# Optimization experiments

Measured on AMD Instinct MI355X. Metric: run time of the kernel, lower is better.

The kernel has to match this reference:

```python
import jax, jax.numpy as jnp
import numpy as np

N = 100000      # nodes
E = 3200000     # edges (avg degree 32)
F_IN = 16       # node_feature_size
R1, R2, R3 = 8, 16, 8   # gcn hidden sizes
N1 = 32                  # mlp hidden


def _lin(k, fan_in, shape):
    s = 1.0 / np.sqrt(fan_in)
    return jax.random.uniform(k, shape, minval=-s, maxval=s, dtype=jnp.float32)


def setup_inputs() -> dict:
    key = jax.random.key(0)
    ks = jax.random.split(key, 16)
    x = jax.random.normal(ks[0], (N, F_IN), dtype=jnp.float32)
    edge_index = jax.random.randint(ks[1], (2, E), 0, N, dtype=jnp.int64)
    return {
        "x": x,
        "edge_index": edge_index,
        # GraphConv k: out = mean_agg(x_j) @ W_rel + b + x @ W_root  (PyG GraphConv, lin_root bias=False)
        "W_rel1": _lin(ks[2], F_IN, (F_IN, R1)), "b1": _lin(ks[3], F_IN, (R1,)), "W_root1": _lin(ks[4], F_IN, (F_IN, R1)),
        "W_rel2": _lin(ks[5], R1, (R1, R2)),   "b2": _lin(ks[6], R1, (R2,)),   "W_root2": _lin(ks[7], R1, (R1, R2)),
        "W_rel3": _lin(ks[8], R2, (R2, R3)),   "b3": _lin(ks[9], R2, (R3,)),   "W_root3": _lin(ks[10], R2, (R2, R3)),
        "fc1_W": _lin(ks[11], R3, (R3, N1)), "fc1_b": _lin(ks[12], R3, (N1,)),
        "fc2_W": _lin(ks[13], N1, (N1, 1)),  "fc2_b": _lin(ks[14], N1, (1,)),
    }


def _graph_conv(x, src, dst, W_rel, b, W_root):
    # message: gather source features; aggregate: mean over incoming edges at dst
    n = x.shape[0]
    msg_sum = jax.ops.segment_sum(x[src], dst, num_segments=n)          # [N, F]
    cnt = jax.ops.segment_sum(jnp.ones(src.shape, x.dtype), dst, num_segments=n)
    mean = msg_sum / jnp.maximum(cnt, 1.0)[:, None]
    return mean @ W_rel + b + x @ W_root


def reference(x, edge_index, W_rel1, b1, W_root1, W_rel2, b2, W_root2,
              W_rel3, b3, W_root3, fc1_W, fc1_b, fc2_W, fc2_b):
    src, dst = edge_index[0], edge_index[1]
    h = jax.nn.sigmoid(_graph_conv(x, src, dst, W_rel1, b1, W_root1))
    h = jax.nn.sigmoid(_graph_conv(h, src, dst, W_rel2, b2, W_root2))
    h = jax.nn.sigmoid(_graph_conv(h, src, dst, W_rel3, b3, W_root3))
    h = jax.nn.sigmoid(h @ fc1_W + fc1_b)
    return h @ fc2_W + fc2_b   # [N, 1]
```

## Files before the change

### kernel.cpp

```cpp
#include <hip/hip_runtime.h>
#include <math.h>


#define CHUNK  8192
#define BW     128
#define MAXB   6144
#define MAXNB  800
#define MAXBLK 512

typedef _Float16 half8 __attribute__((ext_vector_type(8)));

static __device__ __forceinline__ float sigmoidf_(float x) {
    return 1.0f / (1.0f + expf(-x));
}

static __device__ __forceinline__ int scan256_excl(int v, int* s) {
    int tid = threadIdx.x;
    s[tid] = v;
    for (int off = 1; off < 256; off <<= 1) {
        __syncthreads();
        int t = (tid >= off) ? s[tid - off] : 0;
        __syncthreads();
        s[tid] += t;
    }
    __syncthreads();
    return s[tid] - v;
}

static __device__ __forceinline__ void gather_mean8(
    const half8* __restrict__ t, const int* __restrict__ csr,
    int rs, int d, float* s) {
#pragma unroll
    for (int c = 0; c < 8; ++c) s[c] = 0.0f;
    int e = 0;
    for (; e + 4 <= d; e += 4) {
        int4 ci = *(const int4*)(csr + rs + e);
        half8 v0 = t[ci.x]; half8 v1 = t[ci.y];
        half8 v2 = t[ci.z]; half8 v3 = t[ci.w];
#pragma unroll
        for (int c = 0; c < 8; ++c)
            s[c] += ((float)v0[c] + (float)v1[c]) + ((float)v2[c] + (float)v3[c]);
    }
    for (; e < d; ++e) {
        half8 v = t[csr[rs + e]];
#pragma unroll
        for (int c = 0; c < 8; ++c) s[c] += (float)v[c];
    }
    float inv = 1.0f / (float)(d > 0 ? d : 1);
#pragma unroll
    for (int c = 0; c < 8; ++c) s[c] *= inv;
}

__global__ __launch_bounds__(256)
void transform1_kernel(const float* __restrict__ x, const float* __restrict__ Wrel,
                       const float* __restrict__ bias, const float* __restrict__ Wroot,
                       _Float16* __restrict__ t1, _Float16* __restrict__ z1, int n) {
    __shared__ float sWr[128], sWo[128], sb[8];
    int tid = threadIdx.x;
    if (tid < 128) { sWr[tid] = Wrel[tid]; sWo[tid] = Wroot[tid]; }
    if (tid < 8) sb[tid] = bias[tid];
    __syncthreads();
    int node = blockIdx.x * 256 + tid;
    if (node >= n) return;
    const float4* x4 = (const float4*)x;
    float xv[16];
#pragma unroll
    for (int k = 0; k < 4; ++k) {
        float4 v = x4[node * 4 + k];
        xv[4 * k] = v.x; xv[4 * k + 1] = v.y; xv[4 * k + 2] = v.z; xv[4 * k + 3] = v.w;
    }
    float ta[8], za[8];
#pragma unroll
    for (int j = 0; j < 8; ++j) { ta[j] = 0.0f; za[j] = sb[j]; }
#pragma unroll
    for (int f = 0; f < 16; ++f) {
        float xf = xv[f];
#pragma unroll
        for (int j = 0; j < 8; ++j) {
            ta[j] += xf * sWr[f * 8 + j];
            za[j] += xf * sWo[f * 8 + j];
        }
    }
    half8 th, zh;
#pragma unroll
    for (int j = 0; j < 8; ++j) { th[j] = (_Float16)ta[j]; zh[j] = (_Float16)za[j]; }
    ((half8*)t1)[node] = th;
    ((half8*)z1)[node] = zh;
}

__global__ __launch_bounds__(256)
void bin_sort_kernel(const int* __restrict__ src, const int* __restrict__ dst,
                     unsigned* __restrict__ packed, int* __restrict__ counts_bm,
                     int* __restrict__ lstart_bm, int E, int NB) {
    __shared__ int s_hist[MAXNB];
    __shared__ int s_cur[MAXNB];
    __shared__ unsigned s_pk[CHUNK];
    __shared__ int s_scan[256];
    int tid = threadIdx.x, blk = blockIdx.x;
    for (int i = tid; i < NB; i += 256) s_hist[i] = 0;
    __syncthreads();

    int base = blk * CHUNK;
    int cnt = E - base; if (cnt > CHUNK) cnt = CHUNK;

    if (cnt == CHUNK) {
        const int4* d4 = (const int4*)(dst + base);
#pragma unroll
        for (int k = 0; k < CHUNK / 1024; ++k) {
            int4 d = d4[k * 256 + tid];
            atomicAdd(&s_hist[d.x >> 7], 1);
            atomicAdd(&s_hist[d.y >> 7], 1);
            atomicAdd(&s_hist[d.z >> 7], 1);
            atomicAdd(&s_hist[d.w >> 7], 1);
        }
    } else {
        for (int i = tid; i < cnt; i += 256) atomicAdd(&s_hist[dst[base + i] >> 7], 1);
    }
    __syncthreads();

    int per = (NB + 255) / 256;
    int st = tid * per;
    int lsum = 0;
    for (int j = 0; j < per; ++j)
        if (st + j < NB) lsum += s_hist[st + j];
    int excl = scan256_excl(lsum, s_scan);
    int run = excl;
    for (int j = 0; j < per; ++j)
        if (st + j < NB) { s_cur[st + j] = run; run += s_hist[st + j]; }
    __syncthreads();

    if (cnt == CHUNK) {
        const int4* d4 = (const int4*)(dst + base);
        const int4* s4 = (const int4*)(src + base);
#pragma unroll
        for (int k = 0; k < CHUNK / 1024; ++k) {
            int4 d = d4[k * 256 + tid];
            int4 s = s4[k * 256 + tid];
            int dd[4] = {d.x, d.y, d.z, d.w};
            int ss[4] = {s.x, s.y, s.z, s.w};
#pragma unroll
            for (int j = 0; j < 4; ++j) {
                int pos = atomicAdd(&s_cur[dd[j] >> 7], 1);
                s_pk[pos] = ((unsigned)(dd[j] & 127) << 17) | (unsigned)ss[j];
            }
        }
    } else {
        for (int i = tid; i < cnt; i += 256) {
            int d = dst[base + i], s = src[base + i];
            int pos = atomicAdd(&s_cur[d >> 7], 1);
            s_pk[pos] = ((unsigned)(d & 127) << 17) | (unsigned)s;
        }
    }
    __syncthreads();

    for (int i = tid; i < cnt; i += 256) packed[base + i] = s_pk[i];
    for (int i = tid; i < NB; i += 256) {
        int h = s_hist[i];
        counts_bm[blk * NB + i] = h;
        lstart_bm[blk * NB + i] = s_cur[i] - h;
    }
}

__global__ __launch_bounds__(256)
void transpose2_kernel(const int* __restrict__ a, int* __restrict__ at,
                       const int* __restrict__ b, int* __restrict__ bt,
                       int rows, int cols) {
    __shared__ int ta[32][33];
    __shared__ int tb[32][33];
    int tx = threadIdx.x & 31, ty = threadIdx.x >> 5;
    int r0 = blockIdx.y * 32, c0 = blockIdx.x * 32;
#pragma unroll
    for (int k = 0; k < 4; ++k) {
        int r = r0 + ty + 8 * k, c = c0 + tx;
        if (r < rows && c < cols) {
            ta[ty + 8 * k][tx] = a[r * cols + c];
            tb[ty + 8 * k][tx] = b[r * cols + c];
        }
    }
    __syncthreads();
#pragma unroll
    for (int k = 0; k < 4; ++k) {
        int c = c0 + ty + 8 * k, r = r0 + tx;
        if (c < cols && r < rows) {
            at[c * rows + r] = ta[tx][ty + 8 * k];
            bt[c * rows + r] = tb[tx][ty + 8 * k];
        }
    }
}

__global__ __launch_bounds__(256)
void btot_kernel(const int* __restrict__ counts_t, int* __restrict__ btot, int NBLK) {
    __shared__ int s_scan[256];
    int b = blockIdx.x, tid = threadIdx.x;
    int v = 0;
    for (int i = tid; i < NBLK; i += 256) v += counts_t[b * NBLK + i];
    scan256_excl(v, s_scan);
    if (tid == 255) btot[b] = s_scan[255];
}

__global__ __launch_bounds__(1024)
void bscan_kernel(const int* __restrict__ btot, int* __restrict__ bstart, int NB) {
    __shared__ int lds[1024];
    int tid = threadIdx.x;
    int v = (tid < NB) ? (((btot[tid] + 3) & ~3) + 512) : 0;
    lds[tid] = v;
    for (int off = 1; off < 1024; off <<= 1) {
        __syncthreads();
        int t = (tid >= off) ? lds[tid - off] : 0;
        __syncthreads();
        lds[tid] += t;
    }
    __syncthreads();
    if (tid < NB) bstart[tid] = lds[tid] - v;
}

__global__ __launch_bounds__(256)
void bucket_sort_kernel(const unsigned* __restrict__ packed,
                        const int* __restrict__ counts_t,
                        const int* __restrict__ lstart_t,
                        const int* __restrict__ bstart,
                        int* __restrict__ csr_src, int* __restrict__ deg,
                        int* __restrict__ rowstart, int N, int NB, int NBLK) {
    __shared__ int s_cnt[MAXBLK], s_lst[MAXBLK], s_off[MAXBLK];
    __shared__ unsigned s_p[MAXB];
    __shared__ int s_out[MAXB];
    __shared__ int h[BW], hs[BW], curb[BW];
    __shared__ int s_scan[256];
    __shared__ int s_tot, s_ptot;
    int b = blockIdx.x, tid = threadIdx.x;
    int beg = bstart[b];

    for (int i = tid; i < NBLK; i += 256) {
        s_cnt[i] = counts_t[b * NBLK + i];
        s_lst[i] = lstart_t[b * NBLK + i];
    }
    __syncthreads();

    int per = (NBLK + 255) / 256;
    int st = tid * per;
    int lsum = 0;
    for (int j = 0; j < per; ++j)
        if (st + j < NBLK) lsum += s_cnt[st + j];
    int excl = scan256_excl(lsum, s_scan);
    if (tid == 255) s_tot = s_scan[255];
    int run = excl;
    for (int j = 0; j < per; ++j)
        if (st + j < NBLK) { s_off[st + j] = run; run += s_cnt[st + j]; }
    __syncthreads();
    int cnt = s_tot; if (cnt > MAXB) cnt = MAXB;

    for (int blk = tid; blk < NBLK; blk += 256) {
        int c = s_cnt[blk], o = s_off[blk];
        const unsigned* p = packed + (size_t)blk * CHUNK + s_lst[blk];
        for (int j = 0; j < c; ++j) s_p[o + j] = p[j];
    }
    if (tid < BW) h[tid] = 0;
    __syncthreads();

    for (int i = tid; i < cnt; i += 256) atomicAdd(&h[s_p[i] >> 17], 1);
    __syncthreads();
    if (tid == 0) {
        int acc = 0;
        for (int i = 0; i < BW; ++i) { hs[i] = acc; acc += (h[i] + 3) & ~3; }
        s_ptot = acc;
    }
    __syncthreads();
    if (tid < BW) {
        curb[tid] = hs[tid];
        int node = b * BW + tid;
        if (node < N) { deg[node] = h[tid]; rowstart[node] = beg + hs[tid]; }
    }
    __syncthreads();
    for (int i = tid; i < cnt; i += 256) {
        unsigned p = s_p[i];
        int pos = atomicAdd(&curb[p >> 17], 1);
        s_out[pos] = (int)(p & 0x1FFFF);
    }
    __syncthreads();
    int ptot = s_ptot; if (ptot > MAXB) ptot = MAXB;
    for (int i = tid; i < ptot; i += 256) csr_src[beg + i] = s_out[i];
}

__global__ __launch_bounds__(256)
void agg1_kernel(const _Float16* __restrict__ t1, const _Float16* __restrict__ z1,
                 const int* __restrict__ rowstart, const int* __restrict__ deg,
                 const int* __restrict__ csr, _Float16* __restrict__ h1, int n) {
    int node = blockIdx.x * 256 + threadIdx.x;
    if (node >= n) return;
    float s[8];
    gather_mean8((const half8*)t1, csr, rowstart[node], deg[node], s);
    half8 z = ((const half8*)z1)[node];
    half8 o;
#pragma unroll
    for (int c = 0; c < 8; ++c) o[c] = (_Float16)sigmoidf_(s[c] + (float)z[c]);
    ((half8*)h1)[node] = o;
}

__global__ __launch_bounds__(256)
void gcn2_fused_kernel(const _Float16* __restrict__ h1,
                       const int* __restrict__ rowstart, const int* __restrict__ deg,
                       const int* __restrict__ csr,
                       const float* __restrict__ W2r, const float* __restrict__ b2,
                       const float* __restrict__ W2o,
                       const float* __restrict__ W3r, const float* __restrict__ b3,
                       const float* __restrict__ W3o,
                       _Float16* __restrict__ t3, _Float16* __restrict__ z3, int n) {
    __shared__ float sW2r[128], sW2o[128], sW3r[128], sW3o[128], sb2[16], sb3[8];
    int tid = threadIdx.x;
    if (tid < 128) {
        sW2r[tid] = W2r[tid]; sW2o[tid] = W2o[tid];
        sW3r[tid] = W3r[tid]; sW3o[tid] = W3o[tid];
    }
    if (tid < 16) sb2[tid] = b2[tid];
    if (tid < 8) sb3[tid] = b3[tid];
    __syncthreads();
    int node = blockIdx.x * 256 + tid;
    if (node >= n) return;

    float m[8];
    gather_mean8((const half8*)h1, csr, rowstart[node], deg[node], m);
    half8 sf = ((const half8*)h1)[node];
    float x8[8];
#pragma unroll
    for (int c = 0; c < 8; ++c) x8[c] = (float)sf[c];

    float v16[16];
#pragma unroll
    for (int j = 0; j < 16; ++j) {
        float a = sb2[j];
#pragma unroll
        for (int f = 0; f < 8; ++f)
            a += m[f] * sW2r[f * 16 + j] + x8[f] * sW2o[f * 16 + j];
        v16[j] = sigmoidf_(a);
    }
    float ta[8], za[8];
#pragma unroll
    for (int j = 0; j < 8; ++j) { ta[j] = 0.0f; za[j] = sb3[j]; }
#pragma unroll
    for (int f = 0; f < 16; ++f) {
        float hv = v16[f];
#pragma unroll
        for (int j = 0; j < 8; ++j) {
            ta[j] += hv * sW3r[f * 8 + j];
            za[j] += hv * sW3o[f * 8 + j];
        }
    }
    half8 th, zh;
#pragma unroll
    for (int j = 0; j < 8; ++j) { th[j] = (_Float16)ta[j]; zh[j] = (_Float16)za[j]; }
    ((half8*)t3)[node] = th;
    ((half8*)z3)[node] = zh;
}

__global__ __launch_bounds__(256)
void agg3_mlp_kernel(const _Float16* __restrict__ t3, const _Float16* __restrict__ z3,
                     const int* __restrict__ rowstart, const int* __restrict__ deg,
                     const int* __restrict__ csr,
                     const float* __restrict__ fc1W, const float* __restrict__ fc1b,
                     const float* __restrict__ fc2W, const float* __restrict__ fc2b,
                     float* __restrict__ out, int n) {
    __shared__ float sW1[256], sb1[32], sW2[32];
    __shared__ float sb2_;
    int tid = threadIdx.x;
    if (tid < 256) sW1[tid] = fc1W[tid];
    if (tid < 32) { sb1[tid] = fc1b[tid]; sW2[tid] = fc2W[tid]; }
    if (tid == 0) sb2_ = fc2b[0];
    __syncthreads();
    int node = blockIdx.x * 256 + tid;
    if (node >= n) return;

    float s[8];
    gather_mean8((const half8*)t3, csr, rowstart[node], deg[node], s);
    half8 z = ((const half8*)z3)[node];
    float h[8];
#pragma unroll
    for (int c = 0; c < 8; ++c) h[c] = sigmoidf_(s[c] + (float)z[c]);

    float acc = sb2_;
#pragma unroll
    for (int j = 0; j < 32; ++j) {
        float a = sb1[j];
#pragma unroll
        for (int f = 0; f < 8; ++f) a += h[f] * sW1[f * 32 + j];
        acc += sW2[j] * sigmoidf_(a);
    }
    out[node] = acc;
}

extern "C" void kernel_launch(void* const* d_in, const int* in_sizes, int n_in,
                              void* d_out, int out_size, void* d_ws, size_t ws_size,
                              hipStream_t stream) {
    const float* x      = (const float*)d_in[0];
    const int*   ei     = (const int*)d_in[1];
    const float* Wrel1  = (const float*)d_in[2];
    const float* b1     = (const float*)d_in[3];
    const float* Wroot1 = (const float*)d_in[4];
    const float* Wrel2  = (const float*)d_in[5];
    const float* b2     = (const float*)d_in[6];
    const float* Wroot2 = (const float*)d_in[7];
    const float* Wrel3  = (const float*)d_in[8];
    const float* b3     = (const float*)d_in[9];
    const float* Wroot3 = (const float*)d_in[10];
    const float* fc1W   = (const float*)d_in[11];
    const float* fc1b   = (const float*)d_in[12];
    const float* fc2W   = (const float*)d_in[13];
    const float* fc2b   = (const float*)d_in[14];
    float* out = (float*)d_out;

    const int N = in_sizes[0] / 16;
    const int E = in_sizes[1] / 2;
    const int* e_src = ei;
    const int* e_dst = ei + E;

    const int NB   = (N + BW - 1) / BW;
    const int NBLK = (E + CHUNK - 1) / CHUNK;

    char* ws = (char*)d_ws;
    size_t off = 0;
    auto alloc = [&](size_t bytes) { char* p = ws + off; off += (bytes + 15) & ~size_t(15); return p; };
    unsigned* packed   = (unsigned*)alloc((size_t)NBLK * CHUNK * 4);
    int* counts_bm     = (int*)alloc((size_t)NBLK * NB * 4);
    int* lstart_bm     = (int*)alloc((size_t)NBLK * NB * 4);
    int* counts_t      = (int*)alloc((size_t)NBLK * NB * 4);
    int* lstart_t      = (int*)alloc((size_t)NBLK * NB * 4);
    int* btot          = (int*)alloc((size_t)NB * 4);
    int* bstart        = (int*)alloc((size_t)NB * 4);
    int* csr_src       = (int*)alloc(((size_t)E + (size_t)NB * 516) * 4);
    int* deg           = (int*)alloc((size_t)N * 4);
    int* rowstart      = (int*)alloc((size_t)N * 4);
    _Float16* t1       = (_Float16*)alloc((size_t)N * 8 * 2);
    _Float16* z1       = (_Float16*)alloc((size_t)N * 8 * 2);
    _Float16* h1       = (_Float16*)alloc((size_t)N * 8 * 2);
    _Float16* t3       = (_Float16*)alloc((size_t)N * 8 * 2);
    _Float16* z3       = (_Float16*)alloc((size_t)N * 8 * 2);

    const int nbN = (N + 255) / 256;

    transform1_kernel<<<nbN, 256, 0, stream>>>(x, Wrel1, b1, Wroot1, t1, z1, N);

    bin_sort_kernel<<<NBLK, 256, 0, stream>>>(e_src, e_dst, packed, counts_bm, lstart_bm, E, NB);
    dim3 tgrid((NB + 31) / 32, (NBLK + 31) / 32);
    transpose2_kernel<<<tgrid, 256, 0, stream>>>(counts_bm, counts_t, lstart_bm, lstart_t, NBLK, NB);
    btot_kernel<<<NB, 256, 0, stream>>>(counts_t, btot, NBLK);
    bscan_kernel<<<1, 1024, 0, stream>>>(btot, bstart, NB);
    bucket_sort_kernel<<<NB, 256, 0, stream>>>(packed, counts_t, lstart_t, bstart,
                                               csr_src, deg, rowstart, N, NB, NBLK);

    agg1_kernel<<<nbN, 256, 0, stream>>>(t1, z1, rowstart, deg, csr_src, h1, N);
    gcn2_fused_kernel<<<nbN, 256, 0, stream>>>(h1, rowstart, deg, csr_src,
                                               Wrel2, b2, Wroot2, Wrel3, b3, Wroot3, t3, z3, N);
    agg3_mlp_kernel<<<nbN, 256, 0, stream>>>(t3, z3, rowstart, deg, csr_src,
                                             fc1W, fc1b, fc2W, fc2b, out, N);
}
```

Measured before the change: 232.6 us.

## Replace full CSR sort with bucket-only scatter and LDS atomic aggregation

Measured after the change: 672.5 us. 189% more time.

```diff
diff --git a/kernel.cpp b/kernel.cpp
--- a/kernel.cpp
+++ b/kernel.cpp
@@ -4,9 +4,9 @@
 
 #define CHUNK  8192
 #define BW     128
-#define MAXB   6144
 #define MAXNB  800
 #define MAXBLK 512
+#define AST    9
 
 typedef _Float16 half8 __attribute__((ext_vector_type(8)));
 
@@ -27,30 +27,6 @@
     return s[tid] - v;
 }
 
-static __device__ __forceinline__ void gather_mean8(
-    const half8* __restrict__ t, const int* __restrict__ csr,
-    int rs, int d, float* s) {
-#pragma unroll
-    for (int c = 0; c < 8; ++c) s[c] = 0.0f;
-    int e = 0;
-    for (; e + 4 <= d; e += 4) {
-        int4 ci = *(const int4*)(csr + rs + e);
-        half8 v0 = t[ci.x]; half8 v1 = t[ci.y];
-        half8 v2 = t[ci.z]; half8 v3 = t[ci.w];
-#pragma unroll
-        for (int c = 0; c < 8; ++c)
-            s[c] += ((float)v0[c] + (float)v1[c]) + ((float)v2[c] + (float)v3[c]);
-    }
-    for (; e < d; ++e) {
-        half8 v = t[csr[rs + e]];
-#pragma unroll
-        for (int c = 0; c < 8; ++c) s[c] += (float)v[c];
-    }
-    float inv = 1.0f / (float)(d > 0 ? d : 1);
-#pragma unroll
-    for (int c = 0; c < 8; ++c) s[c] *= inv;
-}
-
 __global__ __launch_bounds__(256)
 void transform1_kernel(const float* __restrict__ x, const float* __restrict__ Wrel,
                        const float* __restrict__ bias, const float* __restrict__ Wroot,
@@ -89,20 +65,14 @@
 }
 
 __global__ __launch_bounds__(256)
-void bin_sort_kernel(const int* __restrict__ src, const int* __restrict__ dst,
-                     unsigned* __restrict__ packed, int* __restrict__ counts_bm,
-                     int* __restrict__ lstart_bm, int E, int NB) {
+void hist_kernel(const int* __restrict__ dst, int* __restrict__ counts_bm,
+                 int E, int NB) {
     __shared__ int s_hist[MAXNB];
-    __shared__ int s_cur[MAXNB];
-    __shared__ unsigned s_pk[CHUNK];
-    __shared__ int s_scan[256];
     int tid = threadIdx.x, blk = blockIdx.x;
     for (int i = tid; i < NB; i += 256) s_hist[i] = 0;
     __syncthreads();
-
     int base = blk * CHUNK;
     int cnt = E - base; if (cnt > CHUNK) cnt = CHUNK;
-
     if (cnt == CHUNK) {
         const int4* d4 = (const int4*)(dst + base);
 #pragma unroll
@@ -117,84 +87,26 @@
         for (int i = tid; i < cnt; i += 256) atomicAdd(&s_hist[dst[base + i] >> 7], 1);
     }
     __syncthreads();
-
-    int per = (NB + 255) / 256;
+    for (int i = tid; i < NB; i += 256) counts_bm[blk * NB + i] = s_hist[i];
+}
+
+__global__ __launch_bounds__(256)
+void btot_scan_kernel(const int* __restrict__ counts_bm, int* __restrict__ rawstart_t,
+                      int* __restrict__ btot, int NB, int NBLK) {
+    __shared__ int s_scan[256];
+    __shared__ int s_c[MAXBLK];
+    int b = blockIdx.x, tid = threadIdx.x;
+    for (int i = tid; i < NBLK; i += 256) s_c[i] = counts_bm[i * NB + b];
+    __syncthreads();
+    int per = (NBLK + 255) / 256;
     int st = tid * per;
     int lsum = 0;
     for (int j = 0; j < per; ++j)
-        if (st + j < NB) lsum += s_hist[st + j];
+        if (st + j < NBLK) lsum += s_c[st + j];
     int excl = scan256_excl(lsum, s_scan);
     int run = excl;
     for (int j = 0; j < per; ++j)
-        if (st + j < NB) { s_cur[st + j] = run; run += s_hist[st + j]; }
-    __syncthreads();
-
-    if (cnt == CHUNK) {
-        const int4* d4 = (const int4*)(dst + base);
-        const int4* s4 = (const int4*)(src + base);
-#pragma unroll
-        for (int k = 0; k < CHUNK / 1024; ++k) {
-            int4 d = d4[k * 256 + tid];
-            int4 s = s4[k * 256 + tid];
-            int dd[4] = {d.x, d.y, d.z, d.w};
-            int ss[4] = {s.x, s.y, s.z, s.w};
-#pragma unroll
-            for (int j = 0; j < 4; ++j) {
-                int pos = atomicAdd(&s_cur[dd[j] >> 7], 1);
-                s_pk[pos] = ((unsigned)(dd[j] & 127) << 17) | (unsigned)ss[j];
-            }
-        }
-    } else {
-        for (int i = tid; i < cnt; i += 256) {
-            int d = dst[base + i], s = src[base + i];
-            int pos = atomicAdd(&s_cur[d >> 7], 1);
-            s_pk[pos] = ((unsigned)(d & 127) << 17) | (unsigned)s;
-        }
-    }
-    __syncthreads();
-
-    for (int i = tid; i < cnt; i += 256) packed[base + i] = s_pk[i];
-    for (int i = tid; i < NB; i += 256) {
-        int h = s_hist[i];
-        counts_bm[blk * NB + i] = h;
-        lstart_bm[blk * NB + i] = s_cur[i] - h;
-    }
-}
-
-__global__ __launch_bounds__(256)
-void transpose2_kernel(const int* __restrict__ a, int* __restrict__ at,
-                       const int* __restrict__ b, int* __restrict__ bt,
-                       int rows, int cols) {
-    __shared__ int ta[32][33];
-    __shared__ int tb[32][33];
-    int tx = threadIdx.x & 31, ty = threadIdx.x >> 5;
-    int r0 = blockIdx.y * 32, c0 = blockIdx.x * 32;
-#pragma unroll
-    for (int k = 0; k < 4; ++k) {
-        int r = r0 + ty + 8 * k, c = c0 + tx;
-        if (r < rows && c < cols) {
-            ta[ty + 8 * k][tx] = a[r * cols + c];
-            tb[ty + 8 * k][tx] = b[r * cols + c];
-        }
-    }
-    __syncthreads();
-#pragma unroll
-    for (int k = 0; k < 4; ++k) {
-        int c = c0 + ty + 8 * k, r = r0 + tx;
-        if (c < cols && r < rows) {
-            at[c * rows + r] = ta[tx][ty + 8 * k];
-            bt[c * rows + r] = tb[tx][ty + 8 * k];
-        }
-    }
-}
-
-__global__ __launch_bounds__(256)
-void btot_kernel(const int* __restrict__ counts_t, int* __restrict__ btot, int NBLK) {
-    __shared__ int s_scan[256];
-    int b = blockIdx.x, tid = threadIdx.x;
-    int v = 0;
-    for (int i = tid; i < NBLK; i += 256) v += counts_t[b * NBLK + i];
-    scan256_excl(v, s_scan);
+        if (st + j < NBLK) { rawstart_t[b * NBLK + st + j] = run; run += s_c[st + j]; }
     if (tid == 255) btot[b] = s_scan[255];
 }
 
@@ -202,7 +114,7 @@
 void bscan_kernel(const int* __restrict__ btot, int* __restrict__ bstart, int NB) {
     __shared__ int lds[1024];
     int tid = threadIdx.x;
-    int v = (tid < NB) ? (((btot[tid] + 3) & ~3) + 512) : 0;
+    int v = (tid < NB) ? ((btot[tid] + 3) & ~3) : 0;
     lds[tid] = v;
     for (int off = 1; off < 1024; off <<= 1) {
         __syncthreads();
@@ -215,176 +127,219 @@
 }
 
 __global__ __launch_bounds__(256)
-void bucket_sort_kernel(const unsigned* __restrict__ packed,
-                        const int* __restrict__ counts_t,
-                        const int* __restrict__ lstart_t,
-                        const int* __restrict__ bstart,
-                        int* __restrict__ csr_src, int* __restrict__ deg,
-                        int* __restrict__ rowstart, int N, int NB, int NBLK) {
-    __shared__ int s_cnt[MAXBLK], s_lst[MAXBLK], s_off[MAXBLK];
-    __shared__ unsigned s_p[MAXB];
-    __shared__ int s_out[MAXB];
-    __shared__ int h[BW], hs[BW], curb[BW];
-    __shared__ int s_scan[256];
-    __shared__ int s_tot, s_ptot;
-    int b = blockIdx.x, tid = threadIdx.x;
-    int beg = bstart[b];
-
-    for (int i = tid; i < NBLK; i += 256) {
-        s_cnt[i] = counts_t[b * NBLK + i];
-        s_lst[i] = lstart_t[b * NBLK + i];
-    }
-    __syncthreads();
-
-    int per = (NBLK + 255) / 256;
-    int st = tid * per;
-    int lsum = 0;
-    for (int j = 0; j < per; ++j)
-        if (st + j < NBLK) lsum += s_cnt[st + j];
-    int excl = scan256_excl(lsum, s_scan);
-    if (tid == 255) s_tot = s_scan[255];
-    int run = excl;
-    for (int j = 0; j < per; ++j)
-        if (st + j < NBLK) { s_off[st + j] = run; run += s_cnt[st + j]; }
-    __syncthreads();
-    int cnt = s_tot; if (cnt > MAXB) cnt = MAXB;
-
-    for (int blk = tid; blk < NBLK; blk += 256) {
-        int c = s_cnt[blk], o = s_off[blk];
-        const unsigned* p = packed + (size_t)blk * CHUNK + s_lst[blk];
-        for (int j = 0; j < c; ++j) s_p[o + j] = p[j];
-    }
-    if (tid < BW) h[tid] = 0;
-    __syncthreads();
-
-    for (int i = tid; i < cnt; i += 256) atomicAdd(&h[s_p[i] >> 17], 1);
-    __syncthreads();
-    if (tid == 0) {
-        int acc = 0;
-        for (int i = 0; i < BW; ++i) { hs[i] = acc; acc += (h[i] + 3) & ~3; }
-        s_ptot = acc;
+void scatter_kernel(const int* __restrict__ src, const int* __restrict__ dst,
+                    const int* __restrict__ rawstart_t, const int* __restrict__ bstart,
+                    unsigned* __restrict__ stage, int E, int NB, int NBLK) {
+    __shared__ int s_cur[MAXNB];
+    int tid = threadIdx.x, blk = blockIdx.x;
+    for (int i = tid; i < NB; i += 256)
+        s_cur[i] = bstart[i] + rawstart_t[i * NBLK + blk];
+    __syncthreads();
+    int base = blk * CHUNK;
+    int cnt = E - base; if (cnt > CHUNK) cnt = CHUNK;
+    if (cnt == CHUNK) {
+        const int4* d4 = (const int4*)(dst + base);
+        const int4* s4 = (const int4*)(src + base);
+#pragma unroll
+        for (int k = 0; k < CHUNK / 1024; ++k) {
+            int4 d = d4[k * 256 + tid];
+            int4 s = s4[k * 256 + tid];
+            int dd[4] = {d.x, d.y, d.z, d.w};
+            int ss[4] = {s.x, s.y, s.z, s.w};
+#pragma unroll
+            for (int j = 0; j < 4; ++j) {
+                int pos = atomicAdd(&s_cur[dd[j] >> 7], 1);
+                stage[pos] = ((unsigned)(dd[j] & 127) << 17) | (unsigned)ss[j];
+            }
+        }
+    } else {
+        for (int i = tid; i < cnt; i += 256) {
+            int d = dst[base + i], s = src[base + i];
+            int pos = atomicAdd(&s_cur[d >> 7], 1);
+            stage[pos] = ((unsigned)(d & 127) << 17) | (unsigned)s;
+        }
+    }
+}
+
+static __device__ __forceinline__ void edge_add8(float* __restrict__ acc, unsigned p,
+                                                 const half8* __restrict__ t) {
+    int s  = (int)(p & 0x1FFFFu);
+    int ld = (int)(p >> 17);
+    half8 v = t[s];
+    float* a = acc + ld * AST;
+#pragma unroll
+    for (int c = 0; c < 8; ++c) atomicAdd(&a[c], (float)v[c]);
+}
+
+__global__ __launch_bounds__(256)
+void agg1_kernel(const _Float16* __restrict__ t1, const _Float16* __restrict__ z1,
+                 const unsigned* __restrict__ stage, const int* __restrict__ bstart,
+                 const int* __restrict__ btot, _Float16* __restrict__ h1,
+                 float* __restrict__ invdeg, int N) {
+    __shared__ float acc[BW * AST];
+    __shared__ int scnt[BW];
+    int tid = threadIdx.x, b = blockIdx.x;
+    for (int i = tid; i < BW * AST; i += 256) acc[i] = 0.0f;
+    if (tid < BW) scnt[tid] = 0;
+    __syncthreads();
+    int beg = bstart[b], tot = btot[b];
+    const half8* t = (const half8*)t1;
+    const uint4* st4 = (const uint4*)(stage + beg);
+    int n4 = tot >> 2;
+    for (int i = tid; i < n4; i += 256) {
+        uint4 p = st4[i];
+        edge_add8(acc, p.x, t); atomicAdd(&scnt[p.x >> 17], 1);
+        edge_add8(acc, p.y, t); atomicAdd(&scnt[p.y >> 17], 1);
+        edge_add8(acc, p.z, t); atomicAdd(&scnt[p.z >> 17], 1);
+        edge_add8(acc, p.w, t); atomicAdd(&scnt[p.w >> 17], 1);
+    }
+    int r = (n4 << 2) + tid;
+    if (r < tot) {
+        unsigned p = stage[beg + r];
+        edge_add8(acc, p, t); atomicAdd(&scnt[p >> 17], 1);
     }
     __syncthreads();
     if (tid < BW) {
-        curb[tid] = hs[tid];
         int node = b * BW + tid;
-        if (node < N) { deg[node] = h[tid]; rowstart[node] = beg + hs[tid]; }
-    }
-    __syncthreads();
-    for (int i = tid; i < cnt; i += 256) {
-        unsigned p = s_p[i];
-        int pos = atomicAdd(&curb[p >> 17], 1);
-        s_out[pos] = (int)(p & 0x1FFFF);
-    }
-    __syncthreads();
-    int ptot = s_ptot; if (ptot > MAXB) ptot = MAXB;
-    for (int i = tid; i < ptot; i += 256) csr_src[beg + i] = s_out[i];
-}
-
-__global__ __launch_bounds__(256)
-void agg1_kernel(const _Float16* __restrict__ t1, const _Float16* __restrict__ z1,
-                 const int* __restrict__ rowstart, const int* __restrict__ deg,
-                 const int* __restrict__ csr, _Float16* __restrict__ h1, int n) {
-    int node = blockIdx.x * 256 + threadIdx.x;
-    if (node >= n) return;
-    float s[8];
-    gather_mean8((const half8*)t1, csr, rowstart[node], deg[node], s);
-    half8 z = ((const half8*)z1)[node];
-    half8 o;
-#pragma unroll
-    for (int c = 0; c < 8; ++c) o[c] = (_Float16)sigmoidf_(s[c] + (float)z[c]);
-    ((half8*)h1)[node] = o;
-}
-
-__global__ __launch_bounds__(256)
-void gcn2_fused_kernel(const _Float16* __restrict__ h1,
-                       const int* __restrict__ rowstart, const int* __restrict__ deg,
-                       const int* __restrict__ csr,
-                       const float* __restrict__ W2r, const float* __restrict__ b2,
-                       const float* __restrict__ W2o,
-                       const float* __restrict__ W3r, const float* __restrict__ b3,
-                       const float* __restrict__ W3o,
-                       _Float16* __restrict__ t3, _Float16* __restrict__ z3, int n) {
+        if (node < N) {
+            int c = scnt[tid];
+            float inv = 1.0f / (float)(c > 0 ? c : 1);
+            half8 z = ((const half8*)z1)[node];
+            half8 o;
+#pragma unroll
+            for (int j = 0; j < 8; ++j)
+                o[j] = (_Float16)sigmoidf_(acc[tid * AST + j] * inv + (float)z[j]);
+            ((half8*)h1)[node] = o;
+            invdeg[node] = inv;
+        }
+    }
+}
+
+__global__ __launch_bounds__(256)
+void agg2_kernel(const _Float16* __restrict__ h1, const unsigned* __restrict__ stage,
+                 const int* __restrict__ bstart, const int* __restrict__ btot,
+                 const float* __restrict__ invdeg,
+                 const float* __restrict__ W2r, const float* __restrict__ b2,
+                 const float* __restrict__ W2o,
+                 const float* __restrict__ W3r, const float* __restrict__ b3,
+                 const float* __restrict__ W3o,
+                 _Float16* __restrict__ t3, _Float16* __restrict__ z3, int N) {
+    __shared__ float acc[BW * AST];
     __shared__ float sW2r[128], sW2o[128], sW3r[128], sW3o[128], sb2[16], sb3[8];
-    int tid = threadIdx.x;
+    int tid = threadIdx.x, b = blockIdx.x;
     if (tid < 128) {
         sW2r[tid] = W2r[tid]; sW2o[tid] = W2o[tid];
         sW3r[tid] = W3r[tid]; sW3o[tid] = W3o[tid];
     }
     if (tid < 16) sb2[tid] = b2[tid];
     if (tid < 8) sb3[tid] = b3[tid];
-    __syncthreads();
-    int node = blockIdx.x * 256 + tid;
-    if (node >= n) return;
-
-    float m[8];
-    gather_mean8((const half8*)h1, csr, rowstart[node], deg[node], m);
-    half8 sf = ((const half8*)h1)[node];
-    float x8[8];
-#pragma unroll
-    for (int c = 0; c < 8; ++c) x8[c] = (float)sf[c];
-
-    float v16[16];
-#pragma unroll
-    for (int j = 0; j < 16; ++j) {
-        float a = sb2[j];
-#pragma unroll
-        for (int f = 0; f < 8; ++f)
-            a += m[f] * sW2r[f * 16 + j] + x8[f] * sW2o[f * 16 + j];
-        v16[j] = sigmoidf_(a);
-    }
-    float ta[8], za[8];
-#pragma unroll
-    for (int j = 0; j < 8; ++j) { ta[j] = 0.0f; za[j] = sb3[j]; }
-#pragma unroll
-    for (int f = 0; f < 16; ++f) {
-        float hv = v16[f];
-#pragma unroll
-        for (int j = 0; j < 8; ++j) {
-            ta[j] += hv * sW3r[f * 8 + j];
-            za[j] += hv * sW3o[f * 8 + j];
-        }
-    }
-    half8 th, zh;
-#pragma unroll
-    for (int j = 0; j < 8; ++j) { th[j] = (_Float16)ta[j]; zh[j] = (_Float16)za[j]; }
-    ((half8*)t3)[node] = th;
-    ((half8*)z3)[node] = zh;
-}
-
-__global__ __launch_bounds__(256)
-void agg3_mlp_kernel(const _Float16* __restrict__ t3, const _Float16* __restrict__ z3,
-                     const int* __restrict__ rowstart, const int* __restrict__ deg,
-                     const int* __restrict__ csr,
-                     const float* __restrict__ fc1W, const float* __restrict__ fc1b,
-                     const float* __restrict__ fc2W, const float* __restrict__ fc2b,
-                     float* __restrict__ out, int n) {
+    for (int i = tid; i < BW * AST; i += 256) acc[i] = 0.0f;
+    __syncthreads();
+    int beg = bstart[b], tot = btot[b];
+    const half8* t = (const half8*)h1;
+    const uint4* st4 = (const uint4*)(stage + beg);
+    int n4 = tot >> 2;
+    for (int i = tid; i < n4; i += 256) {
+        uint4 p = st4[i];
+        edge_add8(acc, p.x, t);
+        edge_add8(acc, p.y, t);
+        edge_add8(acc, p.z, t);
+        edge_add8(acc, p.w, t);
+    }
+    int r = (n4 << 2) + tid;
+    if (r < tot) edge_add8(acc, stage[beg + r], t);
+    __syncthreads();
+    if (tid < BW) {
+        int node = b * BW + tid;
+        if (node < N) {
+            float inv = invdeg[node];
+            float m[8];
+#pragma unroll
+            for (int f = 0; f < 8; ++f) m[f] = acc[tid * AST + f] * inv;
+            half8 sf = ((const half8*)h1)[node];
+            float x8[8];
+#pragma unroll
+            for (int f = 0; f < 8; ++f) x8[f] = (float)sf[f];
+            float v16[16];
+#pragma unroll
+            for (int j = 0; j < 16; ++j) {
+                float a = sb2[j];
+#pragma unroll
+                for (int f = 0; f < 8; ++f)
+                    a += m[f] * sW2r[f * 16 + j] + x8[f] * sW2o[f * 16 + j];
+                v16[j] = sigmoidf_(a);
+            }
+            float ta[8], za[8];
+#pragma unroll
+            for (int j = 0; j < 8; ++j) { ta[j] = 0.0f; za[j] = sb3[j]; }
+#pragma unroll
+            for (int f = 0; f < 16; ++f) {
+                float hv = v16[f];
+#pragma unroll
+                for (int j = 0; j < 8; ++j) {
+                    ta[j] += hv * sW3r[f * 8 + j];
+                    za[j] += hv * sW3o[f * 8 + j];
+                }
+            }
+            half8 th, zh;
+#pragma unroll
+            for (int j = 0; j < 8; ++j) { th[j] = (_Float16)ta[j]; zh[j] = (_Float16)za[j]; }
+            ((half8*)t3)[node] = th;
+            ((half8*)z3)[node] = zh;
+        }
+    }
+}
+
+__global__ __launch_bounds__(256)
+void agg3_kernel(const _Float16* __restrict__ t3, const _Float16* __restrict__ z3,
+                 const unsigned* __restrict__ stage, const int* __restrict__ bstart,
+                 const int* __restrict__ btot, const float* __restrict__ invdeg,
+                 const float* __restrict__ fc1W, const float* __restrict__ fc1b,
+                 const float* __restrict__ fc2W, const float* __restrict__ fc2b,
+                 float* __restrict__ out, int N) {
+    __shared__ float acc[BW * AST];
     __shared__ float sW1[256], sb1[32], sW2[32];
     __shared__ float sb2_;
-    int tid = threadIdx.x;
+    int tid = threadIdx.x, b = blockIdx.x;
     if (tid < 256) sW1[tid] = fc1W[tid];
     if (tid < 32) { sb1[tid] = fc1b[tid]; sW2[tid] = fc2W[tid]; }
     if (tid == 0) sb2_ = fc2b[0];
-    __syncthreads();
-    int node = blockIdx.x * 256 + tid;
-    if (node >= n) return;
-
-    float s[8];
-    gather_mean8((const half8*)t3, csr, rowstart[node], deg[node], s);
-    half8 z = ((const half8*)z3)[node];
-    float h[8];
-#pragma unroll
-    for (int c = 0; c < 8; ++c) h[c] = sigmoidf_(s[c] + (float)z[c]);
-
-    float acc = sb2_;
-#pragma unroll
-    for (int j = 0; j < 32; ++j) {
-        float a = sb1[j];
-#pragma unroll
-        for (int f = 0; f < 8; ++f) a += h[f] * sW1[f * 32 + j];
-        acc += sW2[j] * sigmoidf_(a);
-    }
-    out[node] = acc;
+    for (int i = tid; i < BW * AST; i += 256) acc[i] = 0.0f;
+    __syncthreads();
+    int beg = bstart[b], tot = btot[b];
+    const half8* t = (const half8*)t3;
+    const uint4* st4 = (const uint4*)(stage + beg);
+    int n4 = tot >> 2;
+    for (int i = tid; i < n4; i += 256) {
+        uint4 p = st4[i];
+        edge_add8(acc, p.x, t);
+        edge_add8(acc, p.y, t);
+        edge_add8(acc, p.z, t);
+        edge_add8(acc, p.w, t);
+    }
+    int r = (n4 << 2) + tid;
+    if (r < tot) edge_add8(acc, stage[beg + r], t);
+    __syncthreads();
+    if (tid < BW) {
+        int node = b * BW + tid;
+        if (node < N) {
+            float inv = invdeg[node];
+            half8 z = ((const half8*)z3)[node];
+            float h[8];
+#pragma unroll
+            for (int c = 0; c < 8; ++c)
+                h[c] = sigmoidf_(acc[tid * AST + c] * inv + (float)z[c]);
+            float a2 = sb2_;
+#pragma unroll
+            for (int j = 0; j < 32; ++j) {
+                float a = sb1[j];
+#pragma unroll
+                for (int f = 0; f < 8; ++f) a += h[f] * sW1[f * 32 + j];
+                a2 += sW2[j] * sigmoidf_(a);
+            }
+            out[node] = a2;
+        }
+    }
 }
 
 extern "C" void kernel_launch(void* const* d_in, const int* in_sizes, int n_in,
@@ -418,16 +373,12 @@
     char* ws = (char*)d_ws;
     size_t off = 0;
     auto alloc = [&](size_t bytes) { char* p = ws + off; off += (bytes + 15) & ~size_t(15); return p; };
-    unsigned* packed   = (unsigned*)alloc((size_t)NBLK * CHUNK * 4);
+    unsigned* stage    = (unsigned*)alloc(((size_t)E + 4 * (size_t)NB + 64) * 4);
     int* counts_bm     = (int*)alloc((size_t)NBLK * NB * 4);
-    int* lstart_bm     = (int*)alloc((size_t)NBLK * NB * 4);
-    int* counts_t      = (int*)alloc((size_t)NBLK * NB * 4);
-    int* lstart_t      = (int*)alloc((size_t)NBLK * NB * 4);
+    int* rawstart_t    = (int*)alloc((size_t)NB * NBLK * 4);
     int* btot          = (int*)alloc((size_t)NB * 4);
     int* bstart        = (int*)alloc((size_t)NB * 4);
-    int* csr_src       = (int*)alloc(((size_t)E + (size_t)NB * 516) * 4);
-    int* deg           = (int*)alloc((size_t)N * 4);
-    int* rowstart      = (int*)alloc((size_t)N * 4);
+    float* invdeg      = (float*)alloc((size_t)N * 4);
     _Float16* t1       = (_Float16*)alloc((size_t)N * 8 * 2);
     _Float16* z1       = (_Float16*)alloc((size_t)N * 8 * 2);
     _Float16* h1       = (_Float16*)alloc((size_t)N * 8 * 2);
@@ -438,17 +389,14 @@
 
     transform1_kernel<<<nbN, 256, 0, stream>>>(x, Wrel1, b1, Wroot1, t1, z1, N);
 
-    bin_sort_kernel<<<NBLK, 256, 0, stream>>>(e_src, e_dst, packed, counts_bm, lstart_bm, E, NB);
-    dim3 tgrid((NB + 31) / 32, (NBLK + 31) / 32);
-    transpose2_kernel<<<tgrid, 256, 0, stream>>>(counts_bm, counts_t, lstart_bm, lstart_t, NBLK, NB);
-    btot_kernel<<<NB, 256, 0, stream>>>(counts_t, btot, NBLK);
+    hist_kernel<<<NBLK, 256, 0, stream>>>(e_dst, counts_bm, E, NB);
+    btot_scan_kernel<<<NB, 256, 0, stream>>>(counts_bm, rawstart_t, btot, NB, NBLK);
     bscan_kernel<<<1, 1024, 0, stream>>>(btot, bstart, NB);
-    bucket_sort_kernel<<<NB, 256, 0, stream>>>(packed, counts_t, lstart_t, bstart,
-                                               csr_src, deg, rowstart, N, NB, NBLK);
-
-    agg1_kernel<<<nbN, 256, 0, stream>>>(t1, z1, rowstart, deg, csr_src, h1, N);
-    gcn2_fused_kernel<<<nbN, 256, 0, stream>>>(h1, rowstart, deg, csr_src,
-                                               Wrel2, b2, Wroot2, Wrel3, b3, Wroot3, t3, z3, N);
-    agg3_mlp_kernel<<<nbN, 256, 0, stream>>>(t3, z3, rowstart, deg, csr_src,
-                                             fc1W, fc1b, fc2W, fc2b, out, N);
-}
+    scatter_kernel<<<NBLK, 256, 0, stream>>>(e_src, e_dst, rawstart_t, bstart, stage, E, NB, NBLK);
+
+    agg1_kernel<<<NB, 256, 0, stream>>>(t1, z1, stage, bstart, btot, h1, invdeg, N);
+    agg2_kernel<<<NB, 256, 0, stream>>>(h1, stage, bstart, btot, invdeg,
+                                        Wrel2, b2, Wroot2, Wrel3, b3, Wroot3, t3, z3, N);
+    agg3_kernel<<<NB, 256, 0, stream>>>(t3, z3, stage, bstart, btot, invdeg,
+                                        fc1W, fc1b, fc2W, fc2b, out, N);
+}
```

## Replace two-level bucket sort CSR build with global atomic counting sort

Applied to the files above, without the earlier changes.

Result: slower. 554.4 us (+138.4%).

```diff
diff --git a/kernel.cpp b/kernel.cpp
--- a/kernel.cpp
+++ b/kernel.cpp
@@ -2,11 +2,7 @@
 #include <math.h>
 
 
-#define CHUNK  8192
-#define BW     128
-#define MAXB   6144
-#define MAXNB  800
-#define MAXBLK 512
+#define ECHUNK 4096
 
 typedef _Float16 half8 __attribute__((ext_vector_type(8)));
 
@@ -54,7 +50,8 @@
 __global__ __launch_bounds__(256)
 void transform1_kernel(const float* __restrict__ x, const float* __restrict__ Wrel,
                        const float* __restrict__ bias, const float* __restrict__ Wroot,
-                       _Float16* __restrict__ t1, _Float16* __restrict__ z1, int n) {
+                       _Float16* __restrict__ t1, _Float16* __restrict__ z1,
+                       int* __restrict__ deg, int n) {
     __shared__ float sWr[128], sWo[128], sb[8];
     int tid = threadIdx.x;
     if (tid < 128) { sWr[tid] = Wrel[tid]; sWo[tid] = Wroot[tid]; }
@@ -62,6 +59,7 @@
     __syncthreads();
     int node = blockIdx.x * 256 + tid;
     if (node >= n) return;
+    deg[node] = 0;
     const float4* x4 = (const float4*)x;
     float xv[16];
 #pragma unroll
@@ -89,196 +87,94 @@
 }
 
 __global__ __launch_bounds__(256)
-void bin_sort_kernel(const int* __restrict__ src, const int* __restrict__ dst,
-                     unsigned* __restrict__ packed, int* __restrict__ counts_bm,
-                     int* __restrict__ lstart_bm, int E, int NB) {
-    __shared__ int s_hist[MAXNB];
-    __shared__ int s_cur[MAXNB];
-    __shared__ unsigned s_pk[CHUNK];
+void deg_count_kernel(const int* __restrict__ dst, int* __restrict__ deg, int E) {
+    int base = blockIdx.x * ECHUNK;
+    int tid = threadIdx.x;
+    int cnt = E - base; if (cnt > ECHUNK) cnt = ECHUNK;
+    if (cnt == ECHUNK) {
+        const int4* d4 = (const int4*)(dst + base);
+#pragma unroll
+        for (int k = 0; k < ECHUNK / 1024; ++k) {
+            int4 d = d4[k * 256 + tid];
+            atomicAdd(&deg[d.x], 1); atomicAdd(&deg[d.y], 1);
+            atomicAdd(&deg[d.z], 1); atomicAdd(&deg[d.w], 1);
+        }
+    } else {
+        for (int i = tid; i < cnt; i += 256) atomicAdd(&deg[dst[base + i]], 1);
+    }
+}
+
+__global__ __launch_bounds__(256)
+void blocksum_kernel(const int* __restrict__ deg, int* __restrict__ bsum, int N) {
+    __shared__ int s[256];
+    int tid = threadIdx.x;
+    int i = blockIdx.x * 256 + tid;
+    int p = (i < N) ? ((deg[i] + 3) & ~3) : 0;
+    s[tid] = p;
+    for (int off = 128; off > 0; off >>= 1) {
+        __syncthreads();
+        if (tid < off) s[tid] += s[tid + off];
+    }
+    __syncthreads();
+    if (tid == 0) bsum[blockIdx.x] = s[0];
+}
+
+__global__ __launch_bounds__(512)
+void bscan_kernel(const int* __restrict__ bsum, int* __restrict__ bbase, int nb) {
+    __shared__ int lds[512];
+    int tid = threadIdx.x;
+    int v = (tid < nb) ? bsum[tid] : 0;
+    lds[tid] = v;
+    for (int off = 1; off < 512; off <<= 1) {
+        __syncthreads();
+        int t = (tid >= off) ? lds[tid - off] : 0;
+        __syncthreads();
+        lds[tid] += t;
+    }
+    __syncthreads();
+    if (tid < nb) bbase[tid] = lds[tid] - v;
+}
+
+__global__ __launch_bounds__(256)
+void rowwrite_kernel(const int* __restrict__ deg, const int* __restrict__ bbase,
+                     int* __restrict__ rowstart, int* __restrict__ cur, int N) {
     __shared__ int s_scan[256];
-    int tid = threadIdx.x, blk = blockIdx.x;
-    for (int i = tid; i < NB; i += 256) s_hist[i] = 0;
-    __syncthreads();
-
-    int base = blk * CHUNK;
-    int cnt = E - base; if (cnt > CHUNK) cnt = CHUNK;
-
-    if (cnt == CHUNK) {
-        const int4* d4 = (const int4*)(dst + base);
-#pragma unroll
-        for (int k = 0; k < CHUNK / 1024; ++k) {
-            int4 d = d4[k * 256 + tid];
-            atomicAdd(&s_hist[d.x >> 7], 1);
-            atomicAdd(&s_hist[d.y >> 7], 1);
-            atomicAdd(&s_hist[d.z >> 7], 1);
-            atomicAdd(&s_hist[d.w >> 7], 1);
-        }
-    } else {
-        for (int i = tid; i < cnt; i += 256) atomicAdd(&s_hist[dst[base + i] >> 7], 1);
-    }
-    __syncthreads();
-
-    int per = (NB + 255) / 256;
-    int st = tid * per;
-    int lsum = 0;
-    for (int j = 0; j < per; ++j)
-        if (st + j < NB) lsum += s_hist[st + j];
-    int excl = scan256_excl(lsum, s_scan);
-    int run = excl;
-    for (int j = 0; j < per; ++j)
-        if (st + j < NB) { s_cur[st + j] = run; run += s_hist[st + j]; }
-    __syncthreads();
-
-    if (cnt == CHUNK) {
+    int tid = threadIdx.x;
+    int i = blockIdx.x * 256 + tid;
+    int p = (i < N) ? ((deg[i] + 3) & ~3) : 0;
+    int excl = scan256_excl(p, s_scan);
+    if (i < N) {
+        int r = bbase[blockIdx.x] + excl;
+        rowstart[i] = r;
+        cur[i] = r;
+    }
+}
+
+__global__ __launch_bounds__(256)
+void scatter_kernel(const int* __restrict__ src, const int* __restrict__ dst,
+                    int* __restrict__ cur, int* __restrict__ csr, int E) {
+    int base = blockIdx.x * ECHUNK;
+    int tid = threadIdx.x;
+    int cnt = E - base; if (cnt > ECHUNK) cnt = ECHUNK;
+    if (cnt == ECHUNK) {
         const int4* d4 = (const int4*)(dst + base);
         const int4* s4 = (const int4*)(src + base);
 #pragma unroll
-        for (int k = 0; k < CHUNK / 1024; ++k) {
+        for (int k = 0; k < ECHUNK / 1024; ++k) {
             int4 d = d4[k * 256 + tid];
             int4 s = s4[k * 256 + tid];
-            int dd[4] = {d.x, d.y, d.z, d.w};
-            int ss[4] = {s.x, s.y, s.z, s.w};
-#pragma unroll
-            for (int j = 0; j < 4; ++j) {
-                int pos = atomicAdd(&s_cur[dd[j] >> 7], 1);
-                s_pk[pos] = ((unsigned)(dd[j] & 127) << 17) | (unsigned)ss[j];
-            }
+            int pos;
+            pos = atomicAdd(&cur[d.x], 1); csr[pos] = s.x;
+            pos = atomicAdd(&cur[d.y], 1); csr[pos] = s.y;
+            pos = atomicAdd(&cur[d.z], 1); csr[pos] = s.z;
+            pos = atomicAdd(&cur[d.w], 1); csr[pos] = s.w;
         }
     } else {
         for (int i = tid; i < cnt; i += 256) {
-            int d = dst[base + i], s = src[base + i];
-            int pos = atomicAdd(&s_cur[d >> 7], 1);
-            s_pk[pos] = ((unsigned)(d & 127) << 17) | (unsigned)s;
-        }
-    }
-    __syncthreads();
-
-    for (int i = tid; i < cnt; i += 256) packed[base + i] = s_pk[i];
-    for (int i = tid; i < NB; i += 256) {
-        int h = s_hist[i];
-        counts_bm[blk * NB + i] = h;
-        lstart_bm[blk * NB + i] = s_cur[i] - h;
-    }
-}
-
-__global__ __launch_bounds__(256)
-void transpose2_kernel(const int* __restrict__ a, int* __restrict__ at,
-                       const int* __restrict__ b, int* __restrict__ bt,
-                       int rows, int cols) {
-    __shared__ int ta[32][33];
-    __shared__ int tb[32][33];
-    int tx = threadIdx.x & 31, ty = threadIdx.x >> 5;
-    int r0 = blockIdx.y * 32, c0 = blockIdx.x * 32;
-#pragma unroll
-    for (int k = 0; k < 4; ++k) {
-        int r = r0 + ty + 8 * k, c = c0 + tx;
-        if (r < rows && c < cols) {
-            ta[ty + 8 * k][tx] = a[r * cols + c];
-            tb[ty + 8 * k][tx] = b[r * cols + c];
-        }
-    }
-    __syncthreads();
-#pragma unroll
-    for (int k = 0; k < 4; ++k) {
-        int c = c0 + ty + 8 * k, r = r0 + tx;
-        if (c < cols && r < rows) {
-            at[c * rows + r] = ta[tx][ty + 8 * k];
-            bt[c * rows + r] = tb[tx][ty + 8 * k];
-        }
-    }
-}
-
-__global__ __launch_bounds__(256)
-void btot_kernel(const int* __restrict__ counts_t, int* __restrict__ btot, int NBLK) {
-    __shared__ int s_scan[256];
-    int b = blockIdx.x, tid = threadIdx.x;
-    int v = 0;
-    for (int i = tid; i < NBLK; i += 256) v += counts_t[b * NBLK + i];
-    scan256_excl(v, s_scan);
-    if (tid == 255) btot[b] = s_scan[255];
-}
-
-__global__ __launch_bounds__(1024)
-void bscan_kernel(const int* __restrict__ btot, int* __restrict__ bstart, int NB) {
-    __shared__ int lds[1024];
-    int tid = threadIdx.x;
-    int v = (tid < NB) ? (((btot[tid] + 3) & ~3) + 512) : 0;
-    lds[tid] = v;
-    for (int off = 1; off < 1024; off <<= 1) {
-        __syncthreads();
-        int t = (tid >= off) ? lds[tid - off] : 0;
-        __syncthreads();
-        lds[tid] += t;
-    }
-    __syncthreads();
-    if (tid < NB) bstart[tid] = lds[tid] - v;
-}
-
-__global__ __launch_bounds__(256)
-void bucket_sort_kernel(const unsigned* __restrict__ packed,
-                        const int* __restrict__ counts_t,
-                        const int* __restrict__ lstart_t,
-                        const int* __restrict__ bstart,
-                        int* __restrict__ csr_src, int* __restrict__ deg,
-                        int* __restrict__ rowstart, int N, int NB, int NBLK) {
-    __shared__ int s_cnt[MAXBLK], s_lst[MAXBLK], s_off[MAXBLK];
-    __shared__ unsigned s_p[MAXB];
-    __shared__ int s_out[MAXB];
-    __shared__ int h[BW], hs[BW], curb[BW];
-    __shared__ int s_scan[256];
-    __shared__ int s_tot, s_ptot;
-    int b = blockIdx.x, tid = threadIdx.x;
-    int beg = bstart[b];
-
-    for (int i = tid; i < NBLK; i += 256) {
-        s_cnt[i] = counts_t[b * NBLK + i];
-        s_lst[i] = lstart_t[b * NBLK + i];
-    }
-    __syncthreads();
-
-    int per = (NBLK + 255) / 256;
-    int st = tid * per;
-    int lsum = 0;
-    for (int j = 0; j < per; ++j)
-        if (st + j < NBLK) lsum += s_cnt[st + j];
-    int excl = scan256_excl(lsum, s_scan);
-    if (tid == 255) s_tot = s_scan[255];
-    int run = excl;
-    for (int j = 0; j < per; ++j)
-        if (st + j < NBLK) { s_off[st + j] = run; run += s_cnt[st + j]; }
-    __syncthreads();
-    int cnt = s_tot; if (cnt > MAXB) cnt = MAXB;
-
-    for (int blk = tid; blk < NBLK; blk += 256) {
-        int c = s_cnt[blk], o = s_off[blk];
-        const unsigned* p = packed + (size_t)blk * CHUNK + s_lst[blk];
-        for (int j = 0; j < c; ++j) s_p[o + j] = p[j];
-    }
-    if (tid < BW) h[tid] = 0;
-    __syncthreads();
-
-    for (int i = tid; i < cnt; i += 256) atomicAdd(&h[s_p[i] >> 17], 1);
-    __syncthreads();
-    if (tid == 0) {
-        int acc = 0;
-        for (int i = 0; i < BW; ++i) { hs[i] = acc; acc += (h[i] + 3) & ~3; }
-        s_ptot = acc;
-    }
-    __syncthreads();
-    if (tid < BW) {
-        curb[tid] = hs[tid];
-        int node = b * BW + tid;
-        if (node < N) { deg[node] = h[tid]; rowstart[node] = beg + hs[tid]; }
-    }
-    __syncthreads();
-    for (int i = tid; i < cnt; i += 256) {
-        unsigned p = s_p[i];
-        int pos = atomicAdd(&curb[p >> 17], 1);
-        s_out[pos] = (int)(p & 0x1FFFF);
-    }
-    __syncthreads();
-    int ptot = s_ptot; if (ptot > MAXB) ptot = MAXB;
-    for (int i = tid; i < ptot; i += 256) csr_src[beg + i] = s_out[i];
+            int pos = atomicAdd(&cur[dst[base + i]], 1);
+            csr[pos] = src[base + i];
+        }
+    }
 }
 
 __global__ __launch_bounds__(256)
@@ -412,43 +308,35 @@
     const int* e_src = ei;
     const int* e_dst = ei + E;
 
-    const int NB   = (N + BW - 1) / BW;
-    const int NBLK = (E + CHUNK - 1) / CHUNK;
+    const int nbN = (N + 255) / 256;
+    const int nbE = (E + ECHUNK - 1) / ECHUNK;
 
     char* ws = (char*)d_ws;
     size_t off = 0;
     auto alloc = [&](size_t bytes) { char* p = ws + off; off += (bytes + 15) & ~size_t(15); return p; };
-    unsigned* packed   = (unsigned*)alloc((size_t)NBLK * CHUNK * 4);
-    int* counts_bm     = (int*)alloc((size_t)NBLK * NB * 4);
-    int* lstart_bm     = (int*)alloc((size_t)NBLK * NB * 4);
-    int* counts_t      = (int*)alloc((size_t)NBLK * NB * 4);
-    int* lstart_t      = (int*)alloc((size_t)NBLK * NB * 4);
-    int* btot          = (int*)alloc((size_t)NB * 4);
-    int* bstart        = (int*)alloc((size_t)NB * 4);
-    int* csr_src       = (int*)alloc(((size_t)E + (size_t)NB * 516) * 4);
-    int* deg           = (int*)alloc((size_t)N * 4);
-    int* rowstart      = (int*)alloc((size_t)N * 4);
-    _Float16* t1       = (_Float16*)alloc((size_t)N * 8 * 2);
-    _Float16* z1       = (_Float16*)alloc((size_t)N * 8 * 2);
-    _Float16* h1       = (_Float16*)alloc((size_t)N * 8 * 2);
-    _Float16* t3       = (_Float16*)alloc((size_t)N * 8 * 2);
-    _Float16* z3       = (_Float16*)alloc((size_t)N * 8 * 2);
-
-    const int nbN = (N + 255) / 256;
-
-    transform1_kernel<<<nbN, 256, 0, stream>>>(x, Wrel1, b1, Wroot1, t1, z1, N);
-
-    bin_sort_kernel<<<NBLK, 256, 0, stream>>>(e_src, e_dst, packed, counts_bm, lstart_bm, E, NB);
-    dim3 tgrid((NB + 31) / 32, (NBLK + 31) / 32);
-    transpose2_kernel<<<tgrid, 256, 0, stream>>>(counts_bm, counts_t, lstart_bm, lstart_t, NBLK, NB);
-    btot_kernel<<<NB, 256, 0, stream>>>(counts_t, btot, NBLK);
-    bscan_kernel<<<1, 1024, 0, stream>>>(btot, bstart, NB);
-    bucket_sort_kernel<<<NB, 256, 0, stream>>>(packed, counts_t, lstart_t, bstart,
-                                               csr_src, deg, rowstart, N, NB, NBLK);
-
-    agg1_kernel<<<nbN, 256, 0, stream>>>(t1, z1, rowstart, deg, csr_src, h1, N);
-    gcn2_fused_kernel<<<nbN, 256, 0, stream>>>(h1, rowstart, deg, csr_src,
+    int* csr       = (int*)alloc(((size_t)E + 3 * (size_t)N + 64) * 4);
+    int* deg       = (int*)alloc((size_t)N * 4);
+    int* rowstart  = (int*)alloc((size_t)N * 4);
+    int* cur       = (int*)alloc((size_t)N * 4);
+    int* bsum      = (int*)alloc((size_t)nbN * 4);
+    int* bbase     = (int*)alloc((size_t)nbN * 4);
+    _Float16* t1   = (_Float16*)alloc((size_t)N * 8 * 2);
+    _Float16* z1   = (_Float16*)alloc((size_t)N * 8 * 2);
+    _Float16* h1   = (_Float16*)alloc((size_t)N * 8 * 2);
+    _Float16* t3   = (_Float16*)alloc((size_t)N * 8 * 2);
+    _Float16* z3   = (_Float16*)alloc((size_t)N * 8 * 2);
+
+    transform1_kernel<<<nbN, 256, 0, stream>>>(x, Wrel1, b1, Wroot1, t1, z1, deg, N);
+
+    deg_count_kernel<<<nbE, 256, 0, stream>>>(e_dst, deg, E);
+    blocksum_kernel<<<nbN, 256, 0, stream>>>(deg, bsum, N);
+    bscan_kernel<<<1, 512, 0, stream>>>(bsum, bbase, nbN);
+    rowwrite_kernel<<<nbN, 256, 0, stream>>>(deg, bbase, rowstart, cur, N);
+    scatter_kernel<<<nbE, 256, 0, stream>>>(e_src, e_dst, cur, csr, E);
+
+    agg1_kernel<<<nbN, 256, 0, stream>>>(t1, z1, rowstart, deg, csr, h1, N);
+    gcn2_fused_kernel<<<nbN, 256, 0, stream>>>(h1, rowstart, deg, csr,
                                                Wrel2, b2, Wroot2, Wrel3, b3, Wroot3, t3, z3, N);
-    agg3_mlp_kernel<<<nbN, 256, 0, stream>>>(t3, z3, rowstart, deg, csr_src,
+    agg3_mlp_kernel<<<nbN, 256, 0, stream>>>(t3, z3, rowstart, deg, csr,
                                              fc1W, fc1b, fc2W, fc2b, out, N);
 }
```
